# Kernel tuning notes

Hardware: AMD Instinct MI355X
Metric: run time of the kernel (lower is better)

The kernel has to match this reference:

```python
import jax, jax.numpy as jnp
import numpy as np

K = 3            # mc_sampling_steps
ALPHA = 0.5      # importance-weight decay
LAMBDA_COV = 0.5
EPS = 1e-8


def setup_inputs() -> dict:
    key = jax.random.key(0)
    k1, k2, k3, k4 = jax.random.split(key, 4)
    B, S, Et, Es, Ht, Hs = 8, 4096, 128, 16, 2048, 1024
    tg = jax.random.uniform(k1, (B, S, Et)) + 1e-3
    tg = tg / tg.sum(-1, keepdims=True)          # teacher gate probs
    sg = jax.random.uniform(k2, (B, S, Es)) + 1e-3
    sg = sg / sg.sum(-1, keepdims=True)          # student gate probs
    th = jax.random.normal(k3, (B, S, Ht))
    sh = jax.random.normal(k4, (B, S, Hs))
    am = jnp.ones((B, S), dtype=jnp.int32)       # all tokens valid
    return {"teacher_gates": tg, "student_gates": sg,
            "teacher_hidden_states": th, "student_hidden_states": sh,
            "attention_mask": am}


def _method_a(teacher_gates, student_gates, attention_mask):
    B, S, Et = teacher_gates.shape
    Es = student_gates.shape[-1]
    N = B * S
    tp = teacher_gates.reshape(N, Et)                 # flat teacher probs [N, Et]
    sp = student_gates.reshape(N, Es)                 # flat student probs [N, Es]
    log_sp = jnp.log(sp)
    vm = attention_mask.reshape(N).astype(tp.dtype)   # valid-token mask [N]
    carry_f = Et // Es                                # expert_dist[::carry] stride
    rows = jnp.arange(N)

    def step(carry, _):
        probs, key = carry
        key, sub = jax.random.split(key)
        idx = jax.random.categorical(sub, jnp.log(probs), axis=-1)        # multinomial [N]
        w = jnp.take_along_axis(probs, idx[:, None], axis=1)[:, 0]        # importance wt
        new = probs.at[rows, idx].multiply(ALPHA)                         # damp sampled expert
        new = new / new.sum(-1, keepdims=True)
        return (new, key), (idx, w)

    (_, _), (idxs, ws) = jax.lax.scan(step, (tp, jax.random.key(42)), None, length=K)
    ws = ws * vm[None, :]                             # [K, N]

    # KL(one_hot(idx)[::carry] || student) = -log sp[i, idx//carry] iff idx % carry == 0
    sidx = jnp.clip(idxs // carry_f, 0, Es - 1)
    hit = (idxs % carry_f) == 0
    kl = jnp.where(hit, -log_sp[rows[None, :], sidx], 0.0)                # [K, N]
    total_weight = ws.sum()
    feat_loss = (kl * ws).sum() / jnp.maximum(total_weight, EPS)

    # expert coverage counts (only teacher experts with index < Es contribute)
    in_range = (idxs < Es).astype(tp.dtype)
    t_counts = jnp.zeros(Et, tp.dtype).at[idxs.reshape(-1)].add((ws * in_range).reshape(-1))
    sval = sp[rows[None, :], jnp.clip(idxs, 0, Es - 1)] * in_range * vm[None, :]
    s_counts = jnp.zeros(Et, tp.dtype).at[idxs.reshape(-1)].add(sval.reshape(-1))

    ta = t_counts / t_counts.sum()
    sa = s_counts / s_counts.sum()
    ta = (ta + EPS); ta = ta / ta.sum()
    sa = (sa + EPS); sa = sa / sa.sum()
    coverage_kl = jnp.sum(ta * (jnp.log(ta) - jnp.log(sa))) / Et          # batchmean over Et
    return feat_loss, coverage_kl, feat_loss + LAMBDA_COV * coverage_kl


def reference(teacher_gates, student_gates, teacher_hidden_states, student_hidden_states, attention_mask):
    # enable_method_a=True, enable_method_b=False -> expert_total_loss == method_a_total_loss
    _, _, total = _method_a(teacher_gates, student_gates, attention_mask)
    return total
```

## Files before the change

### kernel.cpp

```cpp
#include <hip/hip_runtime.h>
#include <stdint.h>

#define ET 128
#define ES 16
#define ACC_STRIDE 258
#define ACC_USED 34
#define MAX_REPL 64

__host__ __device__ inline void tf2x32(uint32_t k0, uint32_t k1,
                                       uint32_t& x0, uint32_t& x1) {
  uint32_t ks2 = k0 ^ k1 ^ 0x1BD11BDAu;
  x0 += k0; x1 += k1;
#define TF_ROT(r) { x0 += x1; x1 = (x1 << (r)) | (x1 >> (32 - (r))); x1 ^= x0; }
  TF_ROT(13) TF_ROT(15) TF_ROT(26) TF_ROT(6)
  x0 += k1;  x1 += ks2 + 1u;
  TF_ROT(17) TF_ROT(29) TF_ROT(16) TF_ROT(24)
  x0 += ks2; x1 += k0 + 2u;
  TF_ROT(13) TF_ROT(15) TF_ROT(26) TF_ROT(6)
  x0 += k0;  x1 += k1 + 3u;
  TF_ROT(17) TF_ROT(29) TF_ROT(16) TF_ROT(24)
  x0 += k1;  x1 += ks2 + 4u;
  TF_ROT(13) TF_ROT(15) TF_ROT(26) TF_ROT(6)
  x0 += ks2; x1 += k0 + 5u;
#undef TF_ROT
}

__device__ inline float unif01(uint32_t s0, uint32_t s1, uint32_t j) {
  uint32_t x0 = 0u, x1 = j;
  tf2x32(s0, s1, x0, x1);
  uint32_t bits = x0 ^ x1;
  float f = __uint_as_float((bits >> 9) | 0x3F800000u) - 1.0f;
  const float TINY = 1.17549435e-38f;
  return fmaxf(TINY, f + TINY);
}

__launch_bounds__(256)
__global__ void sample_kernel(const float* __restrict__ tg,
                              const float* __restrict__ sg,
                              const int* __restrict__ am,
                              double* __restrict__ acc, int repl,
                              uint32_t s00, uint32_t s01,
                              uint32_t s10, uint32_t s11,
                              uint32_t s20, uint32_t s21,
                              int N, int total_waves) {
  __shared__ float lds_t[ES], lds_s[ES];
  __shared__ float lds_w[4], lds_kl[4];
  if (threadIdx.x < ES) { lds_t[threadIdx.x] = 0.f; lds_s[threadIdx.x] = 0.f; }
  __syncthreads();

  const int wslot = threadIdx.x >> 6;
  const int wid = blockIdx.x * 4 + wslot;
  const int lane = threadIdx.x & 63;
  const int gl = lane & 15;
  const int gbase = lane & 0x30;

  float sum_w = 0.f, sum_kl = 0.f;

  for (int base = wid * 4; base < N; base += total_waves * 4) {
    const int nr = base + (lane >> 4);
    const int ok = (nr < N);
    const int n = ok ? nr : (N - 1);

    const float* row = tg + (size_t)n * ET + gl * 8;
    float4 pa = *(const float4*)row;
    float4 pb = *(const float4*)(row + 4);
    float p0 = pa.x, p1 = pa.y, p2 = pa.z, p3 = pa.w;
    float p4 = pb.x, p5 = pb.y, p6 = pb.z, p7 = pb.w;
    float sgv = sg[(size_t)n * ES + gl];
    float vm = ok ? (float)am[n] : 0.f;

    float i0 = __frcp_rn(p0), i1 = __frcp_rn(p1), i2 = __frcp_rn(p2), i3 = __frcp_rn(p3);
    float i4 = __frcp_rn(p4), i5 = __frcp_rn(p5), i6 = __frcp_rn(p6), i7 = __frcp_rn(p7);

    float t = 1.0f;
    const uint32_t jb = (uint32_t)n * ET + (uint32_t)(gl * 8);
    const int ebase = gl * 8;

#define STEP(KA, KB, LAST)                                                      \
    {                                                                           \
      float e0 = -__logf(unif01(KA, KB, jb + 0u)) * i0;                         \
      float e1 = -__logf(unif01(KA, KB, jb + 1u)) * i1;                         \
      float e2 = -__logf(unif01(KA, KB, jb + 2u)) * i2;                         \
      float e3 = -__logf(unif01(KA, KB, jb + 3u)) * i3;                         \
      float e4 = -__logf(unif01(KA, KB, jb + 4u)) * i4;                         \
      float e5 = -__logf(unif01(KA, KB, jb + 5u)) * i5;                         \
      float e6 = -__logf(unif01(KA, KB, jb + 6u)) * i6;                         \
      float e7 = -__logf(unif01(KA, KB, jb + 7u)) * i7;                         \
      unsigned long long key, ko;                                               \
      key = ((unsigned long long)__float_as_uint(e0) << 32) | (uint32_t)(ebase + 0); \
      ko  = ((unsigned long long)__float_as_uint(e1) << 32) | (uint32_t)(ebase + 1); \
      if (ko < key) key = ko;                                                   \
      ko  = ((unsigned long long)__float_as_uint(e2) << 32) | (uint32_t)(ebase + 2); \
      if (ko < key) key = ko;                                                   \
      ko  = ((unsigned long long)__float_as_uint(e3) << 32) | (uint32_t)(ebase + 3); \
      if (ko < key) key = ko;                                                   \
      ko  = ((unsigned long long)__float_as_uint(e4) << 32) | (uint32_t)(ebase + 4); \
      if (ko < key) key = ko;                                                   \
      ko  = ((unsigned long long)__float_as_uint(e5) << 32) | (uint32_t)(ebase + 5); \
      if (ko < key) key = ko;                                                   \
      ko  = ((unsigned long long)__float_as_uint(e6) << 32) | (uint32_t)(ebase + 6); \
      if (ko < key) key = ko;                                                   \
      ko  = ((unsigned long long)__float_as_uint(e7) << 32) | (uint32_t)(ebase + 7); \
      if (ko < key) key = ko;                                                   \
      ko = __shfl_xor(key, 1); if (ko < key) key = ko;                          \
      ko = __shfl_xor(key, 2); if (ko < key) key = ko;                          \
      ko = __shfl_xor(key, 4); if (ko < key) key = ko;                          \
      ko = __shfl_xor(key, 8); if (ko < key) key = ko;                          \
      const int bi = (int)(key & 0xFFu);            \
      const int wl = bi >> 3, wslt = bi & 7;                                    \
      float pw = p0;                                                            \
      pw = (wslt == 1) ? p1 : pw; pw = (wslt == 2) ? p2 : pw;                   \
      pw = (wslt == 3) ? p3 : pw; pw = (wslt == 4) ? p4 : pw;                   \
      pw = (wslt == 5) ? p5 : pw; pw = (wslt == 6) ? p6 : pw;                   \
      pw = (wslt == 7) ? p7 : pw;                                               \
      float w_abs = __shfl(pw, gbase | wl);          \
      float sgkl = __shfl(sgv, gbase | wl);        \
      float sgcv = __shfl(sgv, gbase | (bi & 15));                              \
      float wsv = w_abs * __frcp_rn(t) * vm;           \
      const bool lead = (gl == 0);                                              \
      sum_w += lead ? wsv : 0.f;                                                \
      float klt = ((bi & 7) == 0) ? (-__logf(sgkl)) * wsv : 0.f;                \
      sum_kl += lead ? klt : 0.f;                                               \
      if (lead && bi < ES) {                                                    \
        atomicAdd(&lds_t[bi], wsv);                                             \
        atomicAdd(&lds_s[bi], sgcv * vm);                                       \
      }                                                                         \
      if (!(LAST)) {                                                            \
        const bool mt = (gl == wl);                                             \
        p0 = (mt && wslt == 0) ? p0 * 0.5f : p0;  i0 = (mt && wslt == 0) ? i0 * 2.0f : i0; \
        p1 = (mt && wslt == 1) ? p1 * 0.5f : p1;  i1 = (mt && wslt == 1) ? i1 * 2.0f : i1; \
        p2 = (mt && wslt == 2) ? p2 * 0.5f : p2;  i2 = (mt && wslt == 2) ? i2 * 2.0f : i2; \
        p3 = (mt && wslt == 3) ? p3 * 0.5f : p3;  i3 = (mt && wslt == 3) ? i3 * 2.0f : i3; \
        p4 = (mt && wslt == 4) ? p4 * 0.5f : p4;  i4 = (mt && wslt == 4) ? i4 * 2.0f : i4; \
        p5 = (mt && wslt == 5) ? p5 * 0.5f : p5;  i5 = (mt && wslt == 5) ? i5 * 2.0f : i5; \
        p6 = (mt && wslt == 6) ? p6 * 0.5f : p6;  i6 = (mt && wslt == 6) ? i6 * 2.0f : i6; \
        p7 = (mt && wslt == 7) ? p7 * 0.5f : p7;  i7 = (mt && wslt == 7) ? i7 * 2.0f : i7; \
        t -= 0.5f * w_abs;                                                      \
      }                                                                         \
    }

    STEP(s00, s01, 0)
    STEP(s10, s11, 0)
    STEP(s20, s21, 1)
#undef STEP
  }

#pragma unroll
  for (int off = 32; off; off >>= 1) {
    sum_w += __shfl_xor(sum_w, off);
    sum_kl += __shfl_xor(sum_kl, off);
  }
  if (lane == 0) { lds_w[wslot] = sum_w; lds_kl[wslot] = sum_kl; }
  __syncthreads();

  double* slot = acc + (size_t)(blockIdx.x % repl) * ACC_STRIDE;
  if (threadIdx.x == 0) {
    atomicAdd(&slot[0], (double)(lds_w[0] + lds_w[1] + lds_w[2] + lds_w[3]));
    atomicAdd(&slot[1], (double)(lds_kl[0] + lds_kl[1] + lds_kl[2] + lds_kl[3]));
  }
  if (threadIdx.x < ES) {
    atomicAdd(&slot[2 + threadIdx.x], (double)lds_t[threadIdx.x]);
    atomicAdd(&slot[2 + ES + threadIdx.x], (double)lds_s[threadIdx.x]);
  }
}

__global__ void finalize_kernel(const double* __restrict__ acc, int repl,
                                float* __restrict__ out) {
  __shared__ double tot[ACC_USED];
  const int tid = threadIdx.x;
  if (tid < ACC_USED) {
    double s = 0.0;
    for (int r = 0; r < repl; ++r) s += acc[(size_t)r * ACC_STRIDE + tid];
    tot[tid] = s;
  }
  __syncthreads();

  const double EPSD = 1e-8;
  double tv = (tid < ES) ? tot[2 + tid] : 0.0;
  double sv = (tid < ES) ? tot[2 + ES + tid] : 0.0;
  double tsum = tv, ssum = sv;
#pragma unroll
  for (int off = 8; off; off >>= 1) {
    tsum += __shfl_xor(tsum, off);
    ssum += __shfl_xor(ssum, off);
  }
  double ta = tv / tsum + EPSD;
  double sa = sv / ssum + EPSD;
  double ta2 = (tid < ES) ? ta : 0.0;
  double sa2 = (tid < ES) ? sa : 0.0;
#pragma unroll
  for (int off = 8; off; off >>= 1) {
    ta2 += __shfl_xor(ta2, off);
    sa2 += __shfl_xor(sa2, off);
  }
  ta2 += (double)(ET - ES) * EPSD;
  sa2 += (double)(ET - ES) * EPSD;
  double tn = ta / ta2, sn = sa / sa2;
  double ci = (tid < ES) ? tn * (log(tn) - log(sn)) : 0.0;
#pragma unroll
  for (int off = 8; off; off >>= 1) ci += __shfl_xor(ci, off);

  if (tid == 0) {
    double ta0 = EPSD / ta2, sa0 = EPSD / sa2;
    double cov = ci + (double)(ET - ES) * ta0 * (log(ta0) - log(sa0));
    cov /= (double)ET;
    double feat = tot[1] / fmax(tot[0], EPSD);
    out[0] = (float)(feat + 0.5 * cov);
  }
}

extern "C" void kernel_launch(void* const* d_in, const int* in_sizes, int n_in,
                              void* d_out, int out_size, void* d_ws, size_t ws_size,
                              hipStream_t stream) {
  const float* tg = (const float*)d_in[0];
  const float* sg = (const float*)d_in[1];
  const int*   am = (const int*)d_in[4];
  const int N = in_sizes[4];

  uint32_t key0 = 0u, key1 = 42u;
  uint32_t subs[3][2];
  for (int k = 0; k < 3; ++k) {
    uint32_t a0 = 0u, a1 = 0u; tf2x32(key0, key1, a0, a1);
    uint32_t b0 = 0u, b1 = 1u; tf2x32(key0, key1, b0, b1);
    subs[k][0] = b0; subs[k][1] = b1;
    key0 = a0; key1 = a1;
  }

  int repl = (int)(ws_size / (ACC_STRIDE * sizeof(double)));
  if (repl > MAX_REPL) repl = MAX_REPL;
  if (repl < 1) repl = 1;

  double* acc = (double*)d_ws;
  hipMemsetAsync(d_ws, 0, (size_t)repl * ACC_STRIDE * sizeof(double), stream);

  int blocks = (N + 15) / 16;
  if (blocks > 2048) blocks = 2048;
  const int total_waves = blocks * 4;

  sample_kernel<<<blocks, 256, 0, stream>>>(
      tg, sg, am, acc, repl,
      subs[0][0], subs[0][1], subs[1][0], subs[1][1], subs[2][0], subs[2][1],
      N, total_waves);
  finalize_kernel<<<1, 64, 0, stream>>>(acc, repl, (float*)d_out);
}
```

Before: 60.67 us.

## Fuse finalize into sampling kernel, prefetch next rows, use alignbit rotate

The separate finalize kernel is folded into the sampling kernel through a last-block-done atomic counter, so one launch is removed. The main loop now software-prefetches the next tile of teacher rows while the current one is processed. Threefry rotations use the amdgcn alignbit builtin, and the block count is halved so each wave handles two iterations. The costs are extra registers for the prefetched rows and a serialized final reduction running in a single block.

New measurement: 52.21 us. 13.9% less time.

```diff
diff --git a/kernel.cpp b/kernel.cpp
--- a/kernel.cpp
+++ b/kernel.cpp
@@ -7,11 +7,19 @@
 #define ACC_USED 34
 #define MAX_REPL 64
 
+__host__ __device__ inline uint32_t rotl32(uint32_t x, int r) {
+#ifdef __HIP_DEVICE_COMPILE__
+  return __builtin_amdgcn_alignbit(x, x, (uint32_t)(32 - r));
+#else
+  return (x << r) | (x >> (32 - r));
+#endif
+}
+
 __host__ __device__ inline void tf2x32(uint32_t k0, uint32_t k1,
                                        uint32_t& x0, uint32_t& x1) {
   uint32_t ks2 = k0 ^ k1 ^ 0x1BD11BDAu;
   x0 += k0; x1 += k1;
-#define TF_ROT(r) { x0 += x1; x1 = (x1 << (r)) | (x1 >> (32 - (r))); x1 ^= x0; }
+#define TF_ROT(r) { x0 += x1; x1 = rotl32(x1, r); x1 ^= x0; }
   TF_ROT(13) TF_ROT(15) TF_ROT(26) TF_ROT(6)
   x0 += k1;  x1 += ks2 + 1u;
   TF_ROT(17) TF_ROT(29) TF_ROT(16) TF_ROT(24)
@@ -38,13 +46,18 @@
 __global__ void sample_kernel(const float* __restrict__ tg,
                               const float* __restrict__ sg,
                               const int* __restrict__ am,
-                              double* __restrict__ acc, int repl,
+                              double* __restrict__ acc,
+                              unsigned int* __restrict__ done,
+                              float* __restrict__ out,
+                              int repl,
                               uint32_t s00, uint32_t s01,
                               uint32_t s10, uint32_t s11,
                               uint32_t s20, uint32_t s21,
                               int N, int total_waves) {
   __shared__ float lds_t[ES], lds_s[ES];
   __shared__ float lds_w[4], lds_kl[4];
+  __shared__ int lds_last;
+  __shared__ double tot[ACC_USED];
   if (threadIdx.x < ES) { lds_t[threadIdx.x] = 0.f; lds_s[threadIdx.x] = 0.f; }
   __syncthreads();
 
@@ -53,97 +66,99 @@
   const int lane = threadIdx.x & 63;
   const int gl = lane & 15;
   const int gbase = lane & 0x30;
+  const int stride = total_waves * 4;
 
   float sum_w = 0.f, sum_kl = 0.f;
 
-  for (int base = wid * 4; base < N; base += total_waves * 4) {
-    const int nr = base + (lane >> 4);
-    const int ok = (nr < N);
-    const int n = ok ? nr : (N - 1);
-
-    const float* row = tg + (size_t)n * ET + gl * 8;
-    float4 pa = *(const float4*)row;
-    float4 pb = *(const float4*)(row + 4);
-    float p0 = pa.x, p1 = pa.y, p2 = pa.z, p3 = pa.w;
-    float p4 = pb.x, p5 = pb.y, p6 = pb.z, p7 = pb.w;
-    float sgv = sg[(size_t)n * ES + gl];
-    float vm = ok ? (float)am[n] : 0.f;
-
-    float i0 = __frcp_rn(p0), i1 = __frcp_rn(p1), i2 = __frcp_rn(p2), i3 = __frcp_rn(p3);
-    float i4 = __frcp_rn(p4), i5 = __frcp_rn(p5), i6 = __frcp_rn(p6), i7 = __frcp_rn(p7);
-
-    float t = 1.0f;
-    const uint32_t jb = (uint32_t)n * ET + (uint32_t)(gl * 8);
-    const int ebase = gl * 8;
-
-#define STEP(KA, KB, LAST)                                                      \
-    {                                                                           \
-      float e0 = -__logf(unif01(KA, KB, jb + 0u)) * i0;                         \
-      float e1 = -__logf(unif01(KA, KB, jb + 1u)) * i1;                         \
-      float e2 = -__logf(unif01(KA, KB, jb + 2u)) * i2;                         \
-      float e3 = -__logf(unif01(KA, KB, jb + 3u)) * i3;                         \
-      float e4 = -__logf(unif01(KA, KB, jb + 4u)) * i4;                         \
-      float e5 = -__logf(unif01(KA, KB, jb + 5u)) * i5;                         \
-      float e6 = -__logf(unif01(KA, KB, jb + 6u)) * i6;                         \
-      float e7 = -__logf(unif01(KA, KB, jb + 7u)) * i7;                         \
-      unsigned long long key, ko;                                               \
-      key = ((unsigned long long)__float_as_uint(e0) << 32) | (uint32_t)(ebase + 0); \
-      ko  = ((unsigned long long)__float_as_uint(e1) << 32) | (uint32_t)(ebase + 1); \
-      if (ko < key) key = ko;                                                   \
-      ko  = ((unsigned long long)__float_as_uint(e2) << 32) | (uint32_t)(ebase + 2); \
-      if (ko < key) key = ko;                                                   \
-      ko  = ((unsigned long long)__float_as_uint(e3) << 32) | (uint32_t)(ebase + 3); \
-      if (ko < key) key = ko;                                                   \
-      ko  = ((unsigned long long)__float_as_uint(e4) << 32) | (uint32_t)(ebase + 4); \
-      if (ko < key) key = ko;                                                   \
-      ko  = ((unsigned long long)__float_as_uint(e5) << 32) | (uint32_t)(ebase + 5); \
-      if (ko < key) key = ko;                                                   \
-      ko  = ((unsigned long long)__float_as_uint(e6) << 32) | (uint32_t)(ebase + 6); \
-      if (ko < key) key = ko;                                                   \
-      ko  = ((unsigned long long)__float_as_uint(e7) << 32) | (uint32_t)(ebase + 7); \
-      if (ko < key) key = ko;                                                   \
-      ko = __shfl_xor(key, 1); if (ko < key) key = ko;                          \
-      ko = __shfl_xor(key, 2); if (ko < key) key = ko;                          \
-      ko = __shfl_xor(key, 4); if (ko < key) key = ko;                          \
-      ko = __shfl_xor(key, 8); if (ko < key) key = ko;                          \
-      const int bi = (int)(key & 0xFFu);            \
-      const int wl = bi >> 3, wslt = bi & 7;                                    \
-      float pw = p0;                                                            \
-      pw = (wslt == 1) ? p1 : pw; pw = (wslt == 2) ? p2 : pw;                   \
-      pw = (wslt == 3) ? p3 : pw; pw = (wslt == 4) ? p4 : pw;                   \
-      pw = (wslt == 5) ? p5 : pw; pw = (wslt == 6) ? p6 : pw;                   \
-      pw = (wslt == 7) ? p7 : pw;                                               \
-      float w_abs = __shfl(pw, gbase | wl);          \
-      float sgkl = __shfl(sgv, gbase | wl);        \
-      float sgcv = __shfl(sgv, gbase | (bi & 15));                              \
-      float wsv = w_abs * __frcp_rn(t) * vm;           \
-      const bool lead = (gl == 0);                                              \
-      sum_w += lead ? wsv : 0.f;                                                \
-      float klt = ((bi & 7) == 0) ? (-__logf(sgkl)) * wsv : 0.f;                \
-      sum_kl += lead ? klt : 0.f;                                               \
-      if (lead && bi < ES) {                                                    \
-        atomicAdd(&lds_t[bi], wsv);                                             \
-        atomicAdd(&lds_s[bi], sgcv * vm);                                       \
-      }                                                                         \
-      if (!(LAST)) {                                                            \
-        const bool mt = (gl == wl);                                             \
-        p0 = (mt && wslt == 0) ? p0 * 0.5f : p0;  i0 = (mt && wslt == 0) ? i0 * 2.0f : i0; \
-        p1 = (mt && wslt == 1) ? p1 * 0.5f : p1;  i1 = (mt && wslt == 1) ? i1 * 2.0f : i1; \
-        p2 = (mt && wslt == 2) ? p2 * 0.5f : p2;  i2 = (mt && wslt == 2) ? i2 * 2.0f : i2; \
-        p3 = (mt && wslt == 3) ? p3 * 0.5f : p3;  i3 = (mt && wslt == 3) ? i3 * 2.0f : i3; \
-        p4 = (mt && wslt == 4) ? p4 * 0.5f : p4;  i4 = (mt && wslt == 4) ? i4 * 2.0f : i4; \
-        p5 = (mt && wslt == 5) ? p5 * 0.5f : p5;  i5 = (mt && wslt == 5) ? i5 * 2.0f : i5; \
-        p6 = (mt && wslt == 6) ? p6 * 0.5f : p6;  i6 = (mt && wslt == 6) ? i6 * 2.0f : i6; \
-        p7 = (mt && wslt == 7) ? p7 * 0.5f : p7;  i7 = (mt && wslt == 7) ? i7 * 2.0f : i7; \
-        t -= 0.5f * w_abs;                                                      \
-      }                                                                         \
+#define LOADT(BASE, P, SGV, VM)                                              \
+  {                                                                          \
+    int nr_ = (BASE) + (lane >> 4);                                          \
+    int ok_ = (nr_ < N);                                                     \
+    int n_ = ok_ ? nr_ : (N - 1);                                            \
+    const float4* r4_ = (const float4*)(tg + (size_t)n_ * ET + gl * 8);      \
+    float4 aa_ = r4_[0], bb_ = r4_[1];                                       \
+    P[0] = aa_.x; P[1] = aa_.y; P[2] = aa_.z; P[3] = aa_.w;                  \
+    P[4] = bb_.x; P[5] = bb_.y; P[6] = bb_.z; P[7] = bb_.w;                  \
+    SGV = sg[(size_t)n_ * ES + gl];                                          \
+    VM = ok_ ? (float)am[n_] : 0.f;                                          \
+  }
+
+#define STEP(KA, KB, LAST)                                                   \
+  {                                                                          \
+    float e[8];                                                              \
+    _Pragma("unroll")                                                        \
+    for (int q = 0; q < 8; ++q)                                              \
+      e[q] = -__logf(unif01(KA, KB, jb + (uint32_t)q)) * inv[q];             \
+    unsigned long long key = ~0ull, ko;                                      \
+    _Pragma("unroll")                                                        \
+    for (int q = 0; q < 8; ++q) {                                            \
+      ko = ((unsigned long long)__float_as_uint(e[q]) << 32)                 \
+           | (uint32_t)(ebase + q);                                          \
+      if (ko < key) key = ko;                                                \
+    }                                                                        \
+    ko = __shfl_xor(key, 1); if (ko < key) key = ko;                         \
+    ko = __shfl_xor(key, 2); if (ko < key) key = ko;                         \
+    ko = __shfl_xor(key, 4); if (ko < key) key = ko;                         \
+    ko = __shfl_xor(key, 8); if (ko < key) key = ko;                         \
+    const int bi = (int)(key & 0xFFu);                                       \
+    const int wl = bi >> 3, wslt = bi & 7;                                   \
+    float pw = p[0];                                                         \
+    _Pragma("unroll")                                                        \
+    for (int q = 1; q < 8; ++q) pw = (wslt == q) ? p[q] : pw;                \
+    float w_abs = __shfl(pw, gbase | wl);                                    \
+    float sgkl = __shfl(sgv, gbase | wl);                                    \
+    float sgcv = __shfl(sgv, gbase | (bi & 15));                             \
+    float wsv = w_abs * __frcp_rn(t) * vm;                                   \
+    const bool lead = (gl == 0);                                             \
+    sum_w += lead ? wsv : 0.f;                                               \
+    float klt = ((bi & 7) == 0) ? (-__logf(sgkl)) * wsv : 0.f;               \
+    sum_kl += lead ? klt : 0.f;                                              \
+    if (lead && bi < ES) {                                                   \
+      atomicAdd(&lds_t[bi], wsv);                                            \
+      atomicAdd(&lds_s[bi], sgcv * vm);                                      \
+    }                                                                        \
+    if (!(LAST)) {                                                           \
+      const bool mt = (gl == wl);                                            \
+      _Pragma("unroll")                                                      \
+      for (int q = 0; q < 8; ++q) {                                          \
+        bool hit = mt && (wslt == q);                                        \
+        p[q] = hit ? p[q] * 0.5f : p[q];                                     \
+        inv[q] = hit ? inv[q] * 2.0f : inv[q];                               \
+      }                                                                      \
+      t -= 0.5f * w_abs;                                                     \
+    }                                                                        \
+  }
+
+  float p[8], sgv = 0.f, vm = 0.f;
+  const int base0 = wid * 4;
+  if (base0 < N) LOADT(base0, p, sgv, vm);
+
+  for (int base = base0; base < N; base += stride) {
+    const int nxt = base + stride;
+    float pn[8] = {0, 0, 0, 0, 0, 0, 0, 0};
+    float sgn = 0.f, vmn = 0.f;
+    if (nxt < N) LOADT(nxt, pn, sgn, vmn);
+
+    {
+      int nr = base + (lane >> 4);
+      int n_ = (nr < N) ? nr : (N - 1);
+      const uint32_t jb = (uint32_t)n_ * ET + (uint32_t)(gl * 8);
+      const int ebase = gl * 8;
+      float inv[8];
+#pragma unroll
+      for (int q = 0; q < 8; ++q) inv[q] = __frcp_rn(p[q]);
+      float t = 1.0f;
+      STEP(s00, s01, 0)
+      STEP(s10, s11, 0)
+      STEP(s20, s21, 1)
     }
 
-    STEP(s00, s01, 0)
-    STEP(s10, s11, 0)
-    STEP(s20, s21, 1)
+#pragma unroll
+    for (int q = 0; q < 8; ++q) p[q] = pn[q];
+    sgv = sgn; vm = vmn;
+  }
 #undef STEP
-  }
+#undef LOADT
 
 #pragma unroll
   for (int off = 32; off; off >>= 1) {
@@ -162,16 +177,23 @@
     atomicAdd(&slot[2 + threadIdx.x], (double)lds_t[threadIdx.x]);
     atomicAdd(&slot[2 + ES + threadIdx.x], (double)lds_s[threadIdx.x]);
   }
-}
-
-__global__ void finalize_kernel(const double* __restrict__ acc, int repl,
-                                float* __restrict__ out) {
-  __shared__ double tot[ACC_USED];
+
+  if (threadIdx.x == 0) {
+    __threadfence();
+    unsigned prev = atomicAdd(done, 1u);
+    lds_last = (prev == (unsigned)(gridDim.x - 1)) ? 1 : 0;
+  }
+  __syncthreads();
+  if (!lds_last) return;
+
   const int tid = threadIdx.x;
-  if (tid < ACC_USED) {
-    double s = 0.0;
-    for (int r = 0; r < repl; ++r) s += acc[(size_t)r * ACC_STRIDE + tid];
-    tot[tid] = s;
+  if (tid < ACC_USED) tot[tid] = 0.0;
+  __syncthreads();
+  for (int idx = tid; idx < repl * ACC_USED; idx += 256) {
+    int r = idx / ACC_USED, f = idx - r * ACC_USED;
+    double v = __hip_atomic_load(&acc[(size_t)r * ACC_STRIDE + f],
+                                 __ATOMIC_RELAXED, __HIP_MEMORY_SCOPE_AGENT);
+    atomicAdd(&tot[f], v);
   }
   __syncthreads();
 
@@ -226,20 +248,21 @@
     key0 = a0; key1 = a1;
   }
 
-  int repl = (int)(ws_size / (ACC_STRIDE * sizeof(double)));
+  int repl = (int)((ws_size - 256) / (ACC_STRIDE * sizeof(double)));
   if (repl > MAX_REPL) repl = MAX_REPL;
   if (repl < 1) repl = 1;
 
   double* acc = (double*)d_ws;
-  hipMemsetAsync(d_ws, 0, (size_t)repl * ACC_STRIDE * sizeof(double), stream);
-
-  int blocks = (N + 15) / 16;
+  unsigned int* done = (unsigned int*)((char*)d_ws + (size_t)repl * ACC_STRIDE * sizeof(double));
+  hipMemsetAsync(d_ws, 0, (size_t)repl * ACC_STRIDE * sizeof(double) + 64, stream);
+
+  int blocks = (N + 31) / 32;
   if (blocks > 2048) blocks = 2048;
+  if (blocks < 1) blocks = 1;
   const int total_waves = blocks * 4;
 
   sample_kernel<<<blocks, 256, 0, stream>>>(
-      tg, sg, am, acc, repl,
+      tg, sg, am, acc, done, (float*)d_out, repl,
       subs[0][0], subs[0][1], subs[1][0], subs[1][1], subs[2][0], subs[2][1],
       N, total_waves);
-  finalize_kernel<<<1, 64, 0, stream>>>(acc, repl, (float*)d_out);
-}
+}
```
